# Performance work log

Measured on AMD Instinct MI355X. Metric: run time of the kernel, lower is better.

The kernel has to match this reference:

```python
import jax, jax.numpy as jnp
import numpy as np

B, S, H = 1, 2048, 2048
QL, KVL = 1536, 512
NH, NOPE, ROPE, VD = 16, 128, 64, 128
IH, ID = 16, 128
TOPK = 512
EPS = 1e-6


def _rms_norm(x, g):
    return x * jax.lax.rsqrt(jnp.mean(x * x, -1, keepdims=True) + EPS) * g


def _layer_norm(x, g, b):
    m = jnp.mean(x, -1, keepdims=True)
    v = jnp.mean((x - m) ** 2, -1, keepdims=True)
    return (x - m) * jax.lax.rsqrt(v + EPS) * g + b


def _rope(x, cos, sin):
    # x: [B,S,h,D] (D even), cos/sin: [S,D//2]; neox-style rotate-halves
    x1, x2 = jnp.split(x, 2, -1)
    c = cos[None, :, None, :]
    s = sin[None, :, None, :]
    return jnp.concatenate([x1 * c - x2 * s, x1 * s + x2 * c], -1)


def setup_inputs() -> dict:
    key = jax.random.key(0)
    ks = jax.random.split(key, 10)
    rn = lambda k, sh: (jax.random.normal(k, sh) * 0.02).astype(jnp.float32)
    pos = jnp.arange(S, dtype=jnp.float32)
    inv = 1.0 / (10000.0 ** (jnp.arange(0, ROPE, 2, dtype=jnp.float32) / ROPE))
    ang = pos[:, None] * inv[None, :]  # [S, ROPE//2]
    return {
        "hidden_states": jax.random.normal(ks[0], (B, S, H), jnp.float32),
        "cos": jnp.cos(ang),
        "sin": jnp.sin(ang),
        "Wq_a": rn(ks[1], (H, QL)),
        "q_a_gamma": jnp.ones((QL,), jnp.float32),
        "Wq_b": rn(ks[2], (QL, NH * (NOPE + ROPE))),
        "Wkv_a": rn(ks[3], (H, KVL + ROPE)),
        "kv_a_gamma": jnp.ones((KVL,), jnp.float32),
        "Wkv_b": rn(ks[4], (KVL, NH * (NOPE + VD))),
        "Wo": rn(ks[5], (NH * VD, H)),
        "Wq_idx": rn(ks[6], (QL, IH * ID)),
        "Wk_idx": rn(ks[7], (H, ID)),
        "Ww_idx": rn(ks[8], (H, IH)),
        "kn_gamma": jnp.ones((ID,), jnp.float32),
        "kn_beta": jnp.zeros((ID,), jnp.float32),
        "topk": TOPK,
    }


def reference(hidden_states, cos, sin, Wq_a, q_a_gamma, Wq_b, Wkv_a, kv_a_gamma,
              Wkv_b, Wo, Wq_idx, Wk_idx, Ww_idx, kn_gamma, kn_beta, topk):
    b, s, _ = hidden_states.shape
    softmax_scale = (NOPE + ROPE) ** -0.5

    # ---- low-rank Q path ----
    q_a = _rms_norm(hidden_states @ Wq_a, q_a_gamma)                 # [B,S,QL]
    q = (q_a @ Wq_b).reshape(b, s, NH, NOPE + ROPE)
    q_nope, q_pe = q[..., :NOPE], _rope(q[..., NOPE:], cos, sin)

    # ---- latent KV path (MQA rope key) ----
    kv = hidden_states @ Wkv_a                                        # [B,S,KVL+ROPE]
    kv_c = _rms_norm(kv[..., :KVL], kv_a_gamma)
    k_pe = _rope(kv[..., KVL:][:, :, None, :], cos, sin)[:, :, 0]     # [B,S,ROPE]
    kvb = (kv_c @ Wkv_b).reshape(b, s, NH, NOPE + VD)
    k_nope, v = kvb[..., :NOPE], kvb[..., NOPE:]

    # ---- lightning indexer: I[t,s] = sum_h w[t,h] * relu(q_idx[t,h] . k_idx[s]) ----
    qi = (q_a @ Wq_idx).reshape(b, s, IH, ID)
    qi = jnp.concatenate([_rope(qi[..., :ROPE], cos, sin), qi[..., ROPE:]], -1)
    ki = _layer_norm(hidden_states @ Wk_idx, kn_gamma, kn_beta)       # [B,S,ID]
    ki = jnp.concatenate([_rope(ki[:, :, None, :ROPE], cos, sin)[:, :, 0], ki[..., ROPE:]], -1)
    w = hidden_states @ Ww_idx                                        # [B,S,IH]
    s_h = jax.nn.relu(jnp.einsum('bthd,bsd->bhts', qi, ki)) * (ID ** -0.5)
    idx_scores = jnp.einsum('bth,bhts->bts', w, s_h)                  # [B,S,S]

    causal = jnp.tril(jnp.ones((s, s), bool))
    idx_scores = jnp.where(causal[None], idx_scores, -jnp.inf)
    top_idx = jax.lax.top_k(idx_scores, topk)[1]                      # [B,S,topk]
    sel = jnp.zeros((b, s, s), bool).at[
        jnp.arange(b)[:, None, None], jnp.arange(s)[None, :, None], top_idx
    ].set(True)
    mask = sel & causal[None]                                         # [B,S,S]

    # ---- sparse MLA attention over selected tokens ----
    scores = (jnp.einsum('bthd,bshd->bhts', q_nope, k_nope)
              + jnp.einsum('bthd,bsd->bhts', q_pe, k_pe)) * softmax_scale
    scores = jnp.where(mask[:, None], scores, -jnp.inf)
    attn = jax.nn.softmax(scores, -1)                                 # [B,NH,S,S]
    out = jnp.einsum('bhts,bshd->bthd', attn, v).reshape(b, s, NH * VD)
    return out @ Wo                                                   # [B,S,H]
```

## Files before the change

kernel.cpp:

```cpp
#include <hip/hip_runtime.h>
#include <cstdint>
#include <cstddef>
#include <cmath>

typedef unsigned long long u64;
typedef __attribute__((ext_vector_type(8))) short bf16x8;
typedef __attribute__((ext_vector_type(4))) float f32x4;

static constexpr int S_    = 2048;
static constexpr int H_    = 2048;
static constexpr int TOPKC = 512;

#define SCALE_ATTN 0.07216878364870323f
#define ISCALE_ID  0.08838834764831845f
#define EPS_F 1e-6f

__device__ inline unsigned short f2b(float f) {
  unsigned u = __float_as_uint(f);
  return (unsigned short)((u + 0x7FFFu + ((u >> 16) & 1u)) >> 16);
}
__device__ inline float b2f(unsigned short b) {
  return __uint_as_float(((unsigned)b) << 16);
}
__device__ inline void gload16(const unsigned short* g, unsigned short* l) {
  __builtin_amdgcn_global_load_lds((const __attribute__((address_space(1))) void*)g,
                                   (__attribute__((address_space(3))) void*)l, 16, 0, 0);
}

__global__ __launch_bounds__(256) void k_gemm_bf16(
    const unsigned short* __restrict__ A, int lda,
    const unsigned short* __restrict__ Bt, int K,
    void* __restrict__ C, int ldc, int N, int out_bf16) {
  __shared__ unsigned short As[128 * 64];
  __shared__ unsigned short Bs[128 * 64];
  const int bm = blockIdx.y * 128, bn = blockIdx.x * 128;
  const int tid = threadIdx.x;
  const int lane = tid & 63, w = tid >> 6;
  const int wm = w >> 1, wn = w & 1;
  const int l15 = lane & 15, quarter = lane >> 4;
  const int srow = (lane >> 3), scol = (lane & 7) * 8;

  f32x4 acc[4][4];
#pragma unroll
  for (int i = 0; i < 4; i++)
#pragma unroll
    for (int j = 0; j < 4; j++) acc[i][j] = (f32x4){0.f, 0.f, 0.f, 0.f};

  for (int k0 = 0; k0 < K; k0 += 64) {
    __syncthreads();
#pragma unroll
    for (int i = 0; i < 4; i++) {
      int r0 = w * 32 + i * 8;
      gload16(A  + (size_t)(bm + r0 + srow) * lda + k0 + scol, &As[r0 * 64]);
      gload16(Bt + (size_t)(bn + r0 + srow) * K   + k0 + scol, &Bs[r0 * 64]);
    }
    __syncthreads();
#pragma unroll
    for (int kc = 0; kc < 2; kc++) {
      bf16x8 af[4], bfr[4];
#pragma unroll
      for (int mf = 0; mf < 4; mf++)
        af[mf] = *(const bf16x8*)(As + (wm * 64 + mf * 16 + l15) * 64 + kc * 32 + quarter * 8);
#pragma unroll
      for (int nf = 0; nf < 4; nf++)
        bfr[nf] = *(const bf16x8*)(Bs + (wn * 64 + nf * 16 + l15) * 64 + kc * 32 + quarter * 8);
#pragma unroll
      for (int mf = 0; mf < 4; mf++)
#pragma unroll
        for (int nf = 0; nf < 4; nf++)
          acc[mf][nf] = __builtin_amdgcn_mfma_f32_16x16x32_bf16(af[mf], bfr[nf], acc[mf][nf], 0, 0, 0);
    }
  }
#pragma unroll
  for (int mf = 0; mf < 4; mf++)
#pragma unroll
    for (int nf = 0; nf < 4; nf++)
#pragma unroll
      for (int r = 0; r < 4; r++) {
        int grow = bm + wm * 64 + mf * 16 + quarter * 4 + r;
        int gcol = bn + wn * 64 + nf * 16 + l15;
        if (gcol < N) {
          if (out_bf16) ((unsigned short*)C)[(size_t)grow * ldc + gcol] = f2b(acc[mf][nf][r]);
          else          ((float*)C)[(size_t)grow * ldc + gcol] = acc[mf][nf][r];
        }
      }
}

__global__ __launch_bounds__(256) void k_tcast(const float* __restrict__ W, int K, int N,
                                               unsigned short* __restrict__ Wt) {
  __shared__ float T[32][33];
  int n0 = blockIdx.x * 32, k0 = blockIdx.y * 32;
  int tid = threadIdx.x;
#pragma unroll
  for (int i = 0; i < 4; i++) {
    int idx = tid + 256 * i;
    int r = idx >> 5, c = idx & 31;
    T[r][c] = W[(size_t)(k0 + r) * N + n0 + c];
  }
  __syncthreads();
#pragma unroll
  for (int i = 0; i < 4; i++) {
    int idx = tid + 256 * i;
    int r = idx >> 5, c = idx & 31;
    Wt[(size_t)(n0 + r) * K + k0 + c] = f2b(T[c][r]);
  }
}

__global__ __launch_bounds__(256) void k_tcast16(const float* __restrict__ W, int K,
                                                 unsigned short* __restrict__ Wt) {
  int idx = blockIdx.x * 256 + threadIdx.x;
  if (idx >= K * 16) return;
  int k = idx >> 4, n = idx & 15;
  Wt[(size_t)n * K + k] = f2b(W[(size_t)k * 16 + n]);
}

__global__ __launch_bounds__(256) void k_cast_bf16(const float* __restrict__ in, int pin,
                                                   unsigned short* __restrict__ outp, int pout,
                                                   int rows, int cols) {
  int cols4 = cols >> 2;
  int idx = blockIdx.x * 256 + threadIdx.x;
  if (idx >= rows * cols4) return;
  int r = idx / cols4, c = (idx - r * cols4) * 4;
  const float* ip = in + (size_t)r * pin + c;
  unsigned short* op = outp + (size_t)r * pout + c;
  op[0] = f2b(ip[0]); op[1] = f2b(ip[1]); op[2] = f2b(ip[2]); op[3] = f2b(ip[3]);
}

__global__ __launch_bounds__(256) void k_rmsnorm_cast(
    const float* __restrict__ x, int stride, const float* __restrict__ gamma,
    unsigned short* __restrict__ outp, int n) {
  int r = blockIdx.x;
  const float* p = x + (size_t)r * stride;
  __shared__ float red[256];
  float s = 0.f;
  for (int i = threadIdx.x; i < n; i += 256) { float v = p[i]; s += v * v; }
  red[threadIdx.x] = s; __syncthreads();
  for (int st = 128; st > 0; st >>= 1) { if (threadIdx.x < st) red[threadIdx.x] += red[threadIdx.x + st]; __syncthreads(); }
  float scl = rsqrtf(red[0] / (float)n + EPS_F);
  unsigned short* op = outp + (size_t)r * n;
  for (int i = threadIdx.x; i < n; i += 256) op[i] = f2b(p[i] * scl * gamma[i]);
}

__global__ __launch_bounds__(256) void k_kvfuse(
    const float* __restrict__ fat, int stride, const float* __restrict__ gamma,
    const float* __restrict__ cosb, const float* __restrict__ sinb,
    unsigned short* __restrict__ kvc_b, unsigned short* __restrict__ kpe_b) {
  int t = blockIdx.x, tid = threadIdx.x;
  const float* p = fat + (size_t)t * stride;
  __shared__ float red[256];
  float x0 = p[tid], x1 = p[tid + 256];
  red[tid] = x0 * x0 + x1 * x1; __syncthreads();
  for (int st = 128; st > 0; st >>= 1) { if (tid < st) red[tid] += red[tid + st]; __syncthreads(); }
  float scl = rsqrtf(red[0] * (1.f / 512.f) + EPS_F);
  kvc_b[(size_t)t * 512 + tid]       = f2b(x0 * scl * gamma[tid]);
  kvc_b[(size_t)t * 512 + tid + 256] = f2b(x1 * scl * gamma[tid + 256]);
  if (tid < 32) {
    float a = p[512 + tid], b = p[544 + tid];
    float c = cosb[t * 32 + tid], s = sinb[t * 32 + tid];
    kpe_b[(size_t)t * 64 + tid]      = f2b(a * c - b * s);
    kpe_b[(size_t)t * 64 + 32 + tid] = f2b(a * s + b * c);
  }
}

__global__ __launch_bounds__(128) void k_ki_ln_rope_cast(
    const float* __restrict__ ki, int stride,
    const float* __restrict__ g, const float* __restrict__ b,
    const float* __restrict__ cosb, const float* __restrict__ sinb,
    unsigned short* __restrict__ ko) {
  int t = blockIdx.x, i = threadIdx.x;
  const float* p = ki + (size_t)t * stride;
  __shared__ float red[128];
  __shared__ float buf[128];
  float v = p[i];
  red[i] = v; __syncthreads();
  for (int st = 64; st > 0; st >>= 1) { if (i < st) red[i] += red[i + st]; __syncthreads(); }
  float mean = red[0] * (1.f / 128.f);
  __syncthreads();
  float d = v - mean;
  red[i] = d * d; __syncthreads();
  for (int st = 64; st > 0; st >>= 1) { if (i < st) red[i] += red[i + st]; __syncthreads(); }
  float var = red[0] * (1.f / 128.f);
  float y = d * rsqrtf(var + EPS_F) * g[i] + b[i];
  buf[i] = y; __syncthreads();
  float outv;
  if (i < 32) {
    float c = cosb[t * 32 + i], s = sinb[t * 32 + i];
    outv = buf[i] * c - buf[i + 32] * s;
  } else if (i < 64) {
    int j = i - 32;
    float c = cosb[t * 32 + j], s = sinb[t * 32 + j];
    outv = buf[j] * s + buf[i] * c;
  } else outv = y;
  ko[(size_t)t * 128 + i] = f2b(outv);
}

__global__ __launch_bounds__(256) void k_rope_b(unsigned short* __restrict__ base, int rowstride, int nh,
                                                int hstride, int off, const float* __restrict__ cosb,
                                                const float* __restrict__ sinb, int total) {
  int idx = blockIdx.x * 256 + threadIdx.x;
  if (idx >= total) return;
  int i = idx & 31, h = (idx >> 5) % nh, t = idx / (32 * nh);
  unsigned short* p = base + (size_t)t * rowstride + h * hstride + off;
  float x1 = b2f(p[i]), x2 = b2f(p[i + 32]);
  float c = cosb[t * 32 + i], s = sinb[t * 32 + i];
  p[i] = f2b(x1 * c - x2 * s);
  p[i + 32] = f2b(x1 * s + x2 * c);
}

__global__ __launch_bounds__(256) void k_idx_mfma(
    const unsigned short* __restrict__ qi_b, int qpitch,
    const unsigned short* __restrict__ ki_b,
    const float* __restrict__ wb, int wstride,
    float* __restrict__ out) {
  int bid = blockIdx.x;
  int tb = (int)((sqrtf(8.f * bid + 1.f) - 1.f) * 0.5f);
  while ((tb + 1) * (tb + 2) / 2 <= bid) tb++;
  while (tb * (tb + 1) / 2 > bid) tb--;
  int sb = bid - tb * (tb + 1) / 2;
  int t0 = tb * 64, s0 = sb * 64;

  int tid = threadIdx.x, lane = tid & 63, w = tid >> 6;
  int wm = w >> 1, wn = w & 1;
  int l15 = lane & 15, quarter = lane >> 4;

  __shared__ unsigned short Ks[64 * 128];
  __shared__ unsigned short Qs[2][64 * 128];
  __shared__ float Ws[64][16];

  int srow_[4], scc_[4];
#pragma unroll
  for (int i = 0; i < 4; i++) {
    int row = w * 16 + i * 4 + (lane >> 4);
    int rr = row & 7;
    srow_[i] = row;
    scc_[i] = (lane & 15) ^ rr;
  }
#pragma unroll
  for (int i = 0; i < 4; i++) {
    gload16(ki_b + (size_t)(s0 + srow_[i]) * 128 + scc_[i] * 8, &Ks[(w * 16 + i * 4) * 128]);
    gload16(qi_b + (size_t)(t0 + srow_[i]) * qpitch + scc_[i] * 8, &Qs[0][(w * 16 + i * 4) * 128]);
  }
  for (int i = tid; i < 64 * 16; i += 256) Ws[i >> 4][i & 15] = wb[(size_t)(t0 + (i >> 4)) * wstride + (i & 15)];
  __syncthreads();

  bf16x8 bfr[2][4];
#pragma unroll
  for (int nf = 0; nf < 2; nf++) {
    int row = wn * 32 + nf * 16 + l15;
    int rx = (row & 7) << 3;
#pragma unroll
    for (int kc = 0; kc < 4; kc++)
      bfr[nf][kc] = *(const bf16x8*)(Ks + row * 128 + ((kc * 32 + quarter * 8) ^ rx));
  }

  f32x4 acc[2][2];
#pragma unroll
  for (int mf = 0; mf < 2; mf++)
#pragma unroll
    for (int nf = 0; nf < 2; nf++) acc[mf][nf] = (f32x4){0.f, 0.f, 0.f, 0.f};

  for (int h = 0; h < 16; h++) {
    int cur = h & 1;
    if (h < 15) {
#pragma unroll
      for (int i = 0; i < 4; i++)
        gload16(qi_b + (size_t)(t0 + srow_[i]) * qpitch + (h + 1) * 128 + scc_[i] * 8,
                &Qs[cur ^ 1][(w * 16 + i * 4) * 128]);
    }
    f32x4 acch[2][2];
#pragma unroll
    for (int mf = 0; mf < 2; mf++)
#pragma unroll
      for (int nf = 0; nf < 2; nf++) acch[mf][nf] = (f32x4){0.f, 0.f, 0.f, 0.f};

#pragma unroll
    for (int mf = 0; mf < 2; mf++) {
      int row = wm * 32 + mf * 16 + l15;
      int rx = (row & 7) << 3;
      bf16x8 af[4];
#pragma unroll
      for (int kc = 0; kc < 4; kc++)
        af[kc] = *(const bf16x8*)(Qs[cur] + row * 128 + ((kc * 32 + quarter * 8) ^ rx));
#pragma unroll
      for (int nf = 0; nf < 2; nf++)
#pragma unroll
        for (int kc = 0; kc < 4; kc++)
          acch[mf][nf] = __builtin_amdgcn_mfma_f32_16x16x32_bf16(af[kc], bfr[nf][kc], acch[mf][nf], 0, 0, 0);
    }
#pragma unroll
    for (int mf = 0; mf < 2; mf++) {
#pragma unroll
      for (int r = 0; r < 4; r++) {
        float wv = Ws[wm * 32 + mf * 16 + quarter * 4 + r][h];
#pragma unroll
        for (int nf = 0; nf < 2; nf++)
          acc[mf][nf][r] = fmaf(wv, fmaxf(acch[mf][nf][r], 0.f), acc[mf][nf][r]);
      }
    }
    __syncthreads();
  }
#pragma unroll
  for (int mf = 0; mf < 2; mf++)
#pragma unroll
    for (int nf = 0; nf < 2; nf++)
#pragma unroll
      for (int r = 0; r < 4; r++) {
        int t = t0 + wm * 32 + mf * 16 + quarter * 4 + r;
        int s = s0 + wn * 32 + nf * 16 + l15;
        out[(size_t)t * 2048 + s] = acc[mf][nf][r] * ISCALE_ID;
      }
}

__global__ __launch_bounds__(256) void k_topk_mask(const float* __restrict__ idx_sc, u64* __restrict__ maskw) {
  int t = blockIdx.x;
  int tid = threadIdx.x;
  int n = t + 1;
  if (n <= TOPKC) {
    if (tid < 32) {
      int lo = tid * 64, hi = lo + 63;
      u64 wv;
      if (t >= hi) wv = ~0ULL;
      else if (t < lo) wv = 0ULL;
      else wv = (~0ULL) >> (63 - (t - lo));
      maskw[(size_t)t * 32 + tid] = wv;
    }
    return;
  }
  __shared__ unsigned int u[2048];
  __shared__ int hist[256];
  __shared__ int scan[256];
  __shared__ u64 mw[32];
  __shared__ int sel_b, new_target, tie_base;
  __shared__ int wcnt[4];
  if (tid < 32) mw[tid] = 0ULL;
  const float* row = idx_sc + (size_t)t * 2048;
  for (int s = tid; s < n; s += 256) {
    unsigned int bb = __float_as_uint(row[s]);
    u[s] = (bb & 0x80000000u) ? ~bb : (bb | 0x80000000u);
  }
  __syncthreads();
  unsigned int prefix = 0;
  int target = TOPKC;
  for (int shift = 24; shift >= 0; shift -= 8) {
    hist[tid] = 0;
    __syncthreads();
    unsigned int himask = (shift == 24) ? 0u : (0xFFFFFFFFu << (shift + 8));
    for (int s = tid; s < n; s += 256) {
      unsigned int uv = u[s];
      if ((uv & himask) == prefix) atomicAdd(&hist[(uv >> shift) & 0xFF], 1);
    }
    __syncthreads();
    scan[tid] = hist[tid];
    __syncthreads();
#pragma unroll
    for (int st = 1; st < 256; st <<= 1) {
      int add = (tid + st < 256) ? scan[tid + st] : 0;
      __syncthreads();
      scan[tid] += add;
      __syncthreads();
    }
    int snext = (tid == 255) ? 0 : scan[tid + 1];
    if (scan[tid] >= target && snext < target) { sel_b = tid; new_target = target - snext; }
    __syncthreads();
    prefix |= ((unsigned int)sel_b) << shift;
    target = new_target;
    __syncthreads();
  }
  if (tid == 0) tie_base = 0;
  __syncthreads();
  int wid = tid >> 6, lane = tid & 63;
  for (int s0 = 0; s0 < n; s0 += 256) {
    int s = s0 + tid;
    bool in = (s < n);
    unsigned int uv = in ? u[s] : 0u;
    bool gt = in && (uv > prefix);
    bool tie = in && (uv == prefix);
    u64 bal = __ballot(tie);
    if (lane == 0) wcnt[wid] = __popcll(bal);
    __syncthreads();
    int wbase = tie_base;
    for (int wI = 0; wI < wid; wI++) wbase += wcnt[wI];
    int rank = wbase + __popcll(bal & ((1ULL << lane) - 1ULL));
    bool sel = gt || (tie && rank < target);
    if (sel) atomicOr(&mw[s >> 6], 1ULL << (s & 63));
    __syncthreads();
    if (tid == 0) tie_base += wcnt[0] + wcnt[1] + wcnt[2] + wcnt[3];
    __syncthreads();
  }
  if (tid < 32) maskw[(size_t)t * 32 + tid] = mw[tid];
}

__global__ __launch_bounds__(256) void k_attn_mfma(
    const unsigned short* __restrict__ qb, int qpitch,
    const unsigned short* __restrict__ kvb_b,
    const unsigned short* __restrict__ kpe_b,
    const float* __restrict__ cosb, const float* __restrict__ sinb,
    const u64* __restrict__ maskw,
    unsigned short* __restrict__ attn_b) {
  int ybm = blockIdx.x;
  int h = blockIdx.y;
  int yb = (h < 8) ? ybm : (31 - ybm);
  int t0 = yb * 64;
  int tid = threadIdx.x;
  int lane = tid & 63, wq = tid >> 6;
  int quarter = lane >> 4, l15 = lane & 15;

  __shared__ unsigned short Kd[2][64 * 192];
  __shared__ unsigned short Vts[128 * 64];

  const unsigned short* kb_base[6];
  int kb_step[6];
#pragma unroll
  for (int i = 0; i < 6; i++) {
    int slot = (wq * 6 + i) * 1024 + lane * 16;
    int rowk = slot / 384;
    int coff = slot - rowk * 384;
    int cc = (coff ^ ((rowk & 7) << 4)) >> 4;
    if (cc < 16) { kb_base[i] = kvb_b + (size_t)rowk * 4096 + h * 256 + cc * 8; kb_step[i] = 4096; }
    else         { kb_base[i] = kpe_b + (size_t)rowk * 64 + (cc - 16) * 8;      kb_step[i] = 64; }
  }
  const int vdg = tid & 15, vsp = tid >> 4;
  const unsigned short* vbase = kvb_b + (size_t)(vsp * 4) * 4096 + h * 256 + 128 + vdg * 8;

  bf16x8 qf[6];
  {
    int t = t0 + wq * 16 + l15;
    const unsigned short* qp = qb + (size_t)t * qpitch + h * 192 + quarter * 8;
#pragma unroll
    for (int kc = 0; kc < 6; kc++) qf[kc] = *(const bf16x8*)(qp + kc * 32);
    const float* cp = cosb + t * 32 + quarter * 8;
    const float* sp = sinb + t * 32 + quarter * 8;
    float4 ca = *(const float4*)cp,  cb2 = *(const float4*)(cp + 4);
    float4 sa = *(const float4*)sp,  sb2 = *(const float4*)(sp + 4);
    float carr[8] = {ca.x, ca.y, ca.z, ca.w, cb2.x, cb2.y, cb2.z, cb2.w};
    float sarr[8] = {sa.x, sa.y, sa.z, sa.w, sb2.x, sb2.y, sb2.z, sb2.w};
#pragma unroll
    for (int j = 0; j < 8; j++) {
      float x1 = b2f((unsigned short)qf[4][j]);
      float x2 = b2f((unsigned short)qf[5][j]);
      qf[4][j] = (short)f2b(x1 * carr[j] - x2 * sarr[j]);
      qf[5][j] = (short)f2b(x1 * sarr[j] + x2 * carr[j]);
    }
  }

  f32x4 o[8];
#pragma unroll
  for (int df = 0; df < 8; df++) o[df] = (f32x4){0.f, 0.f, 0.f, 0.f};
  float mcol = -__builtin_inff(), lcol = 0.f;
  const u64* mrow = maskw + (size_t)(t0 + wq * 16 + l15) * 32;
  int nsb = yb + 1;

#pragma unroll
  for (int i = 0; i < 6; i++) gload16(kb_base[i], &Kd[0][(wq * 6 + i) * 512]);
  bf16x8 vr0 = *(const bf16x8*)(vbase);
  bf16x8 vr1 = *(const bf16x8*)(vbase + 4096);
  bf16x8 vr2 = *(const bf16x8*)(vbase + 8192);
  bf16x8 vr3 = *(const bf16x8*)(vbase + 12288);
  __syncthreads();
#pragma unroll
  for (int j = 0; j < 8; j++) {
    int d = vdg * 8 + j;
    uint2 w2;
    w2.x = (unsigned)(unsigned short)vr0[j] | (((unsigned)(unsigned short)vr1[j]) << 16);
    w2.y = (unsigned)(unsigned short)vr2[j] | (((unsigned)(unsigned short)vr3[j]) << 16);
    *(uint2*)((char*)Vts + d * 128 + ((vsp * 8) ^ (((d >> 2) & 7) << 4))) = w2;
  }

  for (int sb = 0; sb < nsb; sb++) {
    int cur = sb & 1;
    __syncthreads();
    bool pf = (sb + 1 < nsb);
    if (pf) {
      size_t s1 = (size_t)(sb + 1) * 64;
#pragma unroll
      for (int i = 0; i < 6; i++)
        gload16(kb_base[i] + s1 * kb_step[i], &Kd[cur ^ 1][(wq * 6 + i) * 512]);
      const unsigned short* vp = vbase + s1 * 4096;
      vr0 = *(const bf16x8*)(vp);
      vr1 = *(const bf16x8*)(vp + 4096);
      vr2 = *(const bf16x8*)(vp + 8192);
      vr3 = *(const bf16x8*)(vp + 12288);
    }
    const unsigned short* Kc = Kd[cur];
    f32x4 sfT[4];
#pragma unroll
    for (int sc = 0; sc < 4; sc++) {
      f32x4 a = (f32x4){0.f, 0.f, 0.f, 0.f};
      int row = sc * 16 + l15;
      int rx = (row & 7) << 4;
#pragma unroll
      for (int kc = 0; kc < 6; kc++) {
        int byte = row * 384 + ((kc * 64 + quarter * 16) ^ rx);
        bf16x8 kf = *(const bf16x8*)((const char*)Kc + byte);
        a = __builtin_amdgcn_mfma_f32_16x16x32_bf16(kf, qf[kc], a, 0, 0, 0);
      }
      sfT[sc] = a;
    }
    u64 w64 = mrow[sb];
    float p[4][4];
#pragma unroll
    for (int sc = 0; sc < 4; sc++)
#pragma unroll
      for (int r = 0; r < 4; r++) {
        int sbit = sc * 16 + quarter * 4 + r;
        bool sel = (w64 >> sbit) & 1ULL;
        p[sc][r] = sel ? sfT[sc][r] * SCALE_ATTN : -__builtin_inff();
      }
    float v = p[0][0];
#pragma unroll
    for (int sc = 0; sc < 4; sc++)
#pragma unroll
      for (int r = 0; r < 4; r++) v = fmaxf(v, p[sc][r]);
    v = fmaxf(v, __shfl_xor(v, 16));
    v = fmaxf(v, __shfl_xor(v, 32));
    float mn = fmaxf(mcol, v);
    bool dead = (mn == -__builtin_inff());
    float scl = dead ? 1.f : __expf(mcol - mn);
#pragma unroll
    for (int sc = 0; sc < 4; sc++)
#pragma unroll
      for (int r = 0; r < 4; r++)
        p[sc][r] = dead ? 0.f : __expf(p[sc][r] - mn);
    mcol = dead ? mcol : mn;
    float rs = 0.f;
#pragma unroll
    for (int sc = 0; sc < 4; sc++)
#pragma unroll
      for (int r = 0; r < 4; r++) rs += p[sc][r];
    rs += __shfl_xor(rs, 16);
    rs += __shfl_xor(rs, 32);
    lcol = lcol * scl + rs;

    unsigned pk[4][2];
#pragma unroll
    for (int sc = 0; sc < 4; sc++)
#pragma unroll
      for (int rr = 0; rr < 2; rr++)
        pk[sc][rr] = (unsigned)f2b(p[sc][2 * rr]) | (((unsigned)f2b(p[sc][2 * rr + 1])) << 16);
    bf16x8 pa[2];
#pragma unroll
    for (int kc = 0; kc < 2; kc++) {
      union { unsigned d[4]; bf16x8 v; } pu;
#pragma unroll
      for (int jj = 0; jj < 4; jj++) {
        int src = ((quarter & 1) * 2 + (jj >> 1)) * 16 + l15;
        unsigned lo = (unsigned)__shfl((int)pk[kc * 2][jj & 1], src);
        unsigned hi = (unsigned)__shfl((int)pk[kc * 2 + 1][jj & 1], src);
        pu.d[jj] = (quarter < 2) ? lo : hi;
      }
      pa[kc] = pu.v;
    }
    float sclr[4];
#pragma unroll
    for (int r = 0; r < 4; r++) sclr[r] = __shfl(scl, quarter * 4 + r);
#pragma unroll
    for (int df = 0; df < 8; df++)
#pragma unroll
      for (int r = 0; r < 4; r++) o[df][r] *= sclr[r];
#pragma unroll
    for (int kc = 0; kc < 2; kc++)
#pragma unroll
      for (int df = 0; df < 8; df++) {
        int d = df * 16 + l15;
        int vbyte = d * 128 + ((kc * 64 + quarter * 16) ^ (((d >> 2) & 7) << 4));
        bf16x8 vf = *(const bf16x8*)((const char*)Vts + vbyte);
        o[df] = __builtin_amdgcn_mfma_f32_16x16x32_bf16(pa[kc], vf, o[df], 0, 0, 0);
      }
    __syncthreads();
    if (pf) {
#pragma unroll
      for (int j = 0; j < 8; j++) {
        int d = vdg * 8 + j;
        uint2 w2;
        w2.x = (unsigned)(unsigned short)vr0[j] | (((unsigned)(unsigned short)vr1[j]) << 16);
        w2.y = (unsigned)(unsigned short)vr2[j] | (((unsigned)(unsigned short)vr3[j]) << 16);
        *(uint2*)((char*)Vts + d * 128 + ((vsp * 8) ^ (((d >> 2) & 7) << 4))) = w2;
      }
    }
  }
  float inv = (lcol > 0.f) ? 1.f / lcol : 0.f;
  float invr[4];
#pragma unroll
  for (int r = 0; r < 4; r++) invr[r] = __shfl(inv, quarter * 4 + r);
#pragma unroll
  for (int r = 0; r < 4; r++) {
    int t = t0 + wq * 16 + quarter * 4 + r;
    unsigned short* op = attn_b + (size_t)t * 2048 + h * 128 + l15;
#pragma unroll
    for (int df = 0; df < 8; df++) op[df * 16] = f2b(o[df][r] * invr[r]);
  }
}

extern "C" void kernel_launch(void* const* d_in, const int* in_sizes, int n_in,
                              void* d_out, int out_size, void* d_ws, size_t ws_size,
                              hipStream_t stream) {
  const float* hs     = (const float*)d_in[0];
  const float* cosb   = (const float*)d_in[1];
  const float* sinb   = (const float*)d_in[2];
  const float* Wq_a   = (const float*)d_in[3];
  const float* q_a_g  = (const float*)d_in[4];
  const float* Wq_b   = (const float*)d_in[5];
  const float* Wkv_a  = (const float*)d_in[6];
  const float* kv_a_g = (const float*)d_in[7];
  const float* Wkv_b  = (const float*)d_in[8];
  const float* Wo     = (const float*)d_in[9];
  const float* Wq_idx = (const float*)d_in[10];
  const float* Wk_idx = (const float*)d_in[11];
  const float* Ww_idx = (const float*)d_in[12];
  const float* kn_g   = (const float*)d_in[13];
  const float* kn_b   = (const float*)d_in[14];
  float* out = (float*)d_out;

  char* base = (char*)d_ws;
  size_t off = 0;
  auto alloc = [&](size_t bytes) { void* p = base + off; off += (bytes + 255) & ~size_t(255); return p; };

  float* fat1 = (float*)alloc((size_t)S_ * 2304 * 4);
  float* idxs = (float*)alloc((size_t)S_ * 2048 * 4);
  unsigned short* attn_b = (unsigned short*)idxs;
  unsigned short* fat2 = (unsigned short*)alloc((size_t)S_ * 5120 * 2);
  u64*   maskw = (u64*)alloc((size_t)S_ * 32 * 8);
  unsigned short* hs_b  = (unsigned short*)alloc((size_t)S_ * 2048 * 2);
  unsigned short* qa_b  = (unsigned short*)alloc((size_t)S_ * 1536 * 2);
  unsigned short* kvc_b = (unsigned short*)alloc((size_t)S_ * 512 * 2);
  unsigned short* kpe_b = (unsigned short*)alloc((size_t)S_ * 64 * 2);
  unsigned short* kvb_b = (unsigned short*)alloc((size_t)S_ * 4096 * 2);
  unsigned short* ki_b  = (unsigned short*)alloc((size_t)S_ * 128 * 2);
  unsigned short* WT    = (unsigned short*)alloc((size_t)5120 * 1536 * 2);

  dim3 blk(256);

  k_cast_bf16<<<dim3((S_ * 2048 / 4) / 256), blk, 0, stream>>>(hs, 2048, hs_b, 2048, S_, 2048);
  k_tcast<<<dim3(1536 / 32, 2048 / 32), blk, 0, stream>>>(Wq_a, 2048, 1536, WT);
  k_tcast<<<dim3(576 / 32, 2048 / 32), blk, 0, stream>>>(Wkv_a, 2048, 576, WT + (size_t)1536 * 2048);
  k_tcast<<<dim3(128 / 32, 2048 / 32), blk, 0, stream>>>(Wk_idx, 2048, 128, WT + (size_t)2112 * 2048);
  k_tcast16<<<dim3((2048 * 16) / 256), blk, 0, stream>>>(Ww_idx, 2048, WT + (size_t)2240 * 2048);
  k_gemm_bf16<<<dim3(18, 16), blk, 0, stream>>>(hs_b, 2048, WT, 2048, fat1, 2304, 2256, 0);
  k_rmsnorm_cast<<<dim3(S_), blk, 0, stream>>>(fat1, 2304, q_a_g, qa_b, 1536);
  k_kvfuse<<<dim3(S_), blk, 0, stream>>>(fat1 + 1536, 2304, kv_a_g, cosb, sinb, kvc_b, kpe_b);
  k_ki_ln_rope_cast<<<dim3(S_), dim3(128), 0, stream>>>(fat1 + 2112, 2304, kn_g, kn_b, cosb, sinb, ki_b);
  k_tcast<<<dim3(3072 / 32, 1536 / 32), blk, 0, stream>>>(Wq_b, 1536, 3072, WT);
  k_tcast<<<dim3(2048 / 32, 1536 / 32), blk, 0, stream>>>(Wq_idx, 1536, 2048, WT + (size_t)3072 * 1536);
  k_gemm_bf16<<<dim3(40, 16), blk, 0, stream>>>(qa_b, 1536, WT, 1536, fat2, 5120, 5120, 1);
  k_rope_b<<<dim3((S_ * 16 * 32) / 256), blk, 0, stream>>>(fat2 + 3072, 5120, 16, 128, 0, cosb, sinb, S_ * 16 * 32);
  k_tcast<<<dim3(4096 / 32, 512 / 32), blk, 0, stream>>>(Wkv_b, 512, 4096, WT);
  k_gemm_bf16<<<dim3(32, 16), blk, 0, stream>>>(kvc_b, 512, WT, 512, kvb_b, 4096, 4096, 1);
  k_idx_mfma<<<dim3(528), blk, 0, stream>>>(fat2 + 3072, 5120, ki_b, fat1 + 2240, 2304, idxs);
  k_topk_mask<<<dim3(S_), blk, 0, stream>>>(idxs, maskw);
  k_attn_mfma<<<dim3(32, 16), blk, 0, stream>>>(fat2, 5120, kvb_b, kpe_b, cosb, sinb, maskw, attn_b);
  k_tcast<<<dim3(2048 / 32, 2048 / 32), blk, 0, stream>>>(Wo, 2048, 2048, WT);
  k_gemm_bf16<<<dim3(16, 16), blk, 0, stream>>>(attn_b, 2048, WT, 2048, out, 2048, 2048, 0);

  (void)in_sizes; (void)n_in; (void)out_size; (void)ws_size;
}
```

Before: 368.0 us.

## Split attention KV range into two partitions with merge; fuse transposes and norms

```diff
diff --git a/kernel.cpp b/kernel.cpp
--- a/kernel.cpp
+++ b/kernel.cpp
@@ -86,32 +86,58 @@
       }
 }
 
-__global__ __launch_bounds__(256) void k_tcast(const float* __restrict__ W, int K, int N,
-                                               unsigned short* __restrict__ Wt) {
-  __shared__ float T[32][33];
-  int n0 = blockIdx.x * 32, k0 = blockIdx.y * 32;
-  int tid = threadIdx.x;
+__device__ inline void tcast_tile(const float* __restrict__ W, int K, int N,
+                                  unsigned short* __restrict__ dst,
+                                  int r, int ntx, int tid, float (*T)[33]) {
+  int xt = r % ntx, kt = r / ntx;
+  int n0 = xt * 32, k0 = kt * 32;
 #pragma unroll
   for (int i = 0; i < 4; i++) {
     int idx = tid + 256 * i;
-    int r = idx >> 5, c = idx & 31;
-    T[r][c] = W[(size_t)(k0 + r) * N + n0 + c];
+    int rr = idx >> 5, c = idx & 31;
+    T[rr][c] = W[(size_t)(k0 + rr) * N + n0 + c];
   }
   __syncthreads();
 #pragma unroll
   for (int i = 0; i < 4; i++) {
     int idx = tid + 256 * i;
-    int r = idx >> 5, c = idx & 31;
-    Wt[(size_t)(n0 + r) * K + k0 + c] = f2b(T[c][r]);
-  }
-}
-
-__global__ __launch_bounds__(256) void k_tcast16(const float* __restrict__ W, int K,
-                                                 unsigned short* __restrict__ Wt) {
-  int idx = blockIdx.x * 256 + threadIdx.x;
-  if (idx >= K * 16) return;
-  int k = idx >> 4, n = idx & 15;
-  Wt[(size_t)n * K + k] = f2b(W[(size_t)k * 16 + n]);
+    int rr = idx >> 5, c = idx & 31;
+    dst[(size_t)(n0 + rr) * K + k0 + c] = f2b(T[c][rr]);
+  }
+}
+
+__global__ __launch_bounds__(256) void k_tcast_p1(
+    const float* __restrict__ Wq_a, const float* __restrict__ Wkv_a,
+    const float* __restrict__ Wk_idx, const float* __restrict__ Ww_idx,
+    unsigned short* __restrict__ WT) {
+  __shared__ float T[32][33];
+  int bid = blockIdx.x, tid = threadIdx.x;
+  if (bid < 3072)      tcast_tile(Wq_a,  2048, 1536, WT,                          bid,        48, tid, T);
+  else if (bid < 4224) tcast_tile(Wkv_a, 2048,  576, WT + (size_t)1536 * 2048,    bid - 3072, 18, tid, T);
+  else if (bid < 4480) tcast_tile(Wk_idx,2048,  128, WT + (size_t)2112 * 2048,    bid - 4224,  4, tid, T);
+  else {
+    int idx = (bid - 4480) * 256 + tid;
+    int k = idx >> 4, n = idx & 15;
+    WT[(size_t)(2240 + n) * 2048 + k] = f2b(Ww_idx[(size_t)k * 16 + n]);
+  }
+}
+
+__global__ __launch_bounds__(256) void k_tcast_p2(
+    const float* __restrict__ Wq_b, const float* __restrict__ Wq_idx,
+    unsigned short* __restrict__ WT) {
+  __shared__ float T[32][33];
+  int bid = blockIdx.x, tid = threadIdx.x;
+  if (bid < 4608) tcast_tile(Wq_b,   1536, 3072, WT,                        bid,        96, tid, T);
+  else            tcast_tile(Wq_idx, 1536, 2048, WT + (size_t)3072 * 1536,  bid - 4608, 64, tid, T);
+}
+
+__global__ __launch_bounds__(256) void k_tcast_p3(
+    const float* __restrict__ Wkv_b, const float* __restrict__ Wo,
+    unsigned short* __restrict__ WT) {
+  __shared__ float T[32][33];
+  int bid = blockIdx.x, tid = threadIdx.x;
+  if (bid < 2048) tcast_tile(Wkv_b,  512, 4096, WT,                       bid,        128, tid, T);
+  else            tcast_tile(Wo,    2048, 2048, WT + (size_t)4096 * 512,  bid - 2048,  64, tid, T);
 }
 
 __global__ __launch_bounds__(256) void k_cast_bf16(const float* __restrict__ in, int pin,
@@ -126,72 +152,63 @@
   op[0] = f2b(ip[0]); op[1] = f2b(ip[1]); op[2] = f2b(ip[2]); op[3] = f2b(ip[3]);
 }
 
-__global__ __launch_bounds__(256) void k_rmsnorm_cast(
-    const float* __restrict__ x, int stride, const float* __restrict__ gamma,
-    unsigned short* __restrict__ outp, int n) {
-  int r = blockIdx.x;
-  const float* p = x + (size_t)r * stride;
-  __shared__ float red[256];
-  float s = 0.f;
-  for (int i = threadIdx.x; i < n; i += 256) { float v = p[i]; s += v * v; }
-  red[threadIdx.x] = s; __syncthreads();
-  for (int st = 128; st > 0; st >>= 1) { if (threadIdx.x < st) red[threadIdx.x] += red[threadIdx.x + st]; __syncthreads(); }
-  float scl = rsqrtf(red[0] / (float)n + EPS_F);
-  unsigned short* op = outp + (size_t)r * n;
-  for (int i = threadIdx.x; i < n; i += 256) op[i] = f2b(p[i] * scl * gamma[i]);
-}
-
-__global__ __launch_bounds__(256) void k_kvfuse(
-    const float* __restrict__ fat, int stride, const float* __restrict__ gamma,
+__global__ __launch_bounds__(256) void k_norms(
+    const float* __restrict__ fat, int stride,
+    const float* __restrict__ qg, const float* __restrict__ kvg,
+    const float* __restrict__ kng, const float* __restrict__ knb,
     const float* __restrict__ cosb, const float* __restrict__ sinb,
-    unsigned short* __restrict__ kvc_b, unsigned short* __restrict__ kpe_b) {
+    unsigned short* __restrict__ qa_b, unsigned short* __restrict__ kvc_b,
+    unsigned short* __restrict__ kpe_b, unsigned short* __restrict__ ki_b) {
   int t = blockIdx.x, tid = threadIdx.x;
   const float* p = fat + (size_t)t * stride;
   __shared__ float red[256];
-  float x0 = p[tid], x1 = p[tid + 256];
-  red[tid] = x0 * x0 + x1 * x1; __syncthreads();
+  __shared__ float buf[128];
+  float x[6]; float s = 0.f;
+#pragma unroll
+  for (int i = 0; i < 6; i++) { x[i] = p[tid + 256 * i]; s += x[i] * x[i]; }
+  red[tid] = s; __syncthreads();
   for (int st = 128; st > 0; st >>= 1) { if (tid < st) red[tid] += red[tid + st]; __syncthreads(); }
-  float scl = rsqrtf(red[0] * (1.f / 512.f) + EPS_F);
-  kvc_b[(size_t)t * 512 + tid]       = f2b(x0 * scl * gamma[tid]);
-  kvc_b[(size_t)t * 512 + tid + 256] = f2b(x1 * scl * gamma[tid + 256]);
+  float scl = rsqrtf(red[0] * (1.f / 1536.f) + EPS_F);
+#pragma unroll
+  for (int i = 0; i < 6; i++)
+    qa_b[(size_t)t * 1536 + tid + 256 * i] = f2b(x[i] * scl * qg[tid + 256 * i]);
+  __syncthreads();
+  float y0 = p[1536 + tid], y1 = p[1792 + tid];
+  red[tid] = y0 * y0 + y1 * y1; __syncthreads();
+  for (int st = 128; st > 0; st >>= 1) { if (tid < st) red[tid] += red[tid + st]; __syncthreads(); }
+  float scl2 = rsqrtf(red[0] * (1.f / 512.f) + EPS_F);
+  kvc_b[(size_t)t * 512 + tid]       = f2b(y0 * scl2 * kvg[tid]);
+  kvc_b[(size_t)t * 512 + 256 + tid] = f2b(y1 * scl2 * kvg[256 + tid]);
   if (tid < 32) {
-    float a = p[512 + tid], b = p[544 + tid];
-    float c = cosb[t * 32 + tid], s = sinb[t * 32 + tid];
-    kpe_b[(size_t)t * 64 + tid]      = f2b(a * c - b * s);
-    kpe_b[(size_t)t * 64 + 32 + tid] = f2b(a * s + b * c);
-  }
-}
-
-__global__ __launch_bounds__(128) void k_ki_ln_rope_cast(
-    const float* __restrict__ ki, int stride,
-    const float* __restrict__ g, const float* __restrict__ b,
-    const float* __restrict__ cosb, const float* __restrict__ sinb,
-    unsigned short* __restrict__ ko) {
-  int t = blockIdx.x, i = threadIdx.x;
-  const float* p = ki + (size_t)t * stride;
-  __shared__ float red[128];
-  __shared__ float buf[128];
-  float v = p[i];
-  red[i] = v; __syncthreads();
-  for (int st = 64; st > 0; st >>= 1) { if (i < st) red[i] += red[i + st]; __syncthreads(); }
+    float a = p[2048 + tid], b = p[2080 + tid];
+    float c = cosb[t * 32 + tid], sn = sinb[t * 32 + tid];
+    kpe_b[(size_t)t * 64 + tid]      = f2b(a * c - b * sn);
+    kpe_b[(size_t)t * 64 + 32 + tid] = f2b(a * sn + b * c);
+  }
+  __syncthreads();
+  float z = (tid < 128) ? p[2112 + tid] : 0.f;
+  red[tid] = z; __syncthreads();
+  for (int st = 128; st > 0; st >>= 1) { if (tid < st) red[tid] += red[tid + st]; __syncthreads(); }
   float mean = red[0] * (1.f / 128.f);
   __syncthreads();
-  float d = v - mean;
-  red[i] = d * d; __syncthreads();
-  for (int st = 64; st > 0; st >>= 1) { if (i < st) red[i] += red[i + st]; __syncthreads(); }
+  float d = (tid < 128) ? (z - mean) : 0.f;
+  red[tid] = d * d; __syncthreads();
+  for (int st = 128; st > 0; st >>= 1) { if (tid < st) red[tid] += red[tid + st]; __syncthreads(); }
   float var = red[0] * (1.f / 128.f);
-  float y = d * rsqrtf(var + EPS_F) * g[i] + b[i];
-  buf[i] = y; __syncthreads();
-  float outv;
-  if (i < 32) {
-    float c = cosb[t * 32 + i], s = sinb[t * 32 + i];
-    outv = buf[i] * c - buf[i + 32] * s;
-  } else if (i < 64) {
-    int j = i - 32;
-    float c = cosb[t * 32 + j], s = sinb[t * 32 + j];
-    outv = buf[j] * s + buf[i] * c;
-  } else outv = y;
-  ko[(size_t)t * 128 + i] = f2b(outv);
+  if (tid < 128) buf[tid] = d * rsqrtf(var + EPS_F) * kng[tid] + knb[tid];
+  __syncthreads();
+  if (tid < 128) {
+    float outv;
+    if (tid < 32) {
+      float c = cosb[t * 32 + tid], sn = sinb[t * 32 + tid];
+      outv = buf[tid] * c - buf[tid + 32] * sn;
+    } else if (tid < 64) {
+      int j = tid - 32;
+      float c = cosb[t * 32 + j], sn = sinb[t * 32 + j];
+      outv = buf[j] * sn + buf[tid] * c;
+    } else outv = buf[tid];
+    ki_b[(size_t)t * 128 + tid] = f2b(outv);
+  }
 }
 
 __global__ __launch_bounds__(256) void k_rope_b(unsigned short* __restrict__ base, int rowstride, int nh,
@@ -231,9 +248,8 @@
 #pragma unroll
   for (int i = 0; i < 4; i++) {
     int row = w * 16 + i * 4 + (lane >> 4);
-    int rr = row & 7;
     srow_[i] = row;
-    scc_[i] = (lane & 15) ^ rr;
+    scc_[i] = (lane & 15) ^ (row & 7);
   }
 #pragma unroll
   for (int i = 0; i < 4; i++) {
@@ -273,6 +289,7 @@
 #pragma unroll
       for (int nf = 0; nf < 2; nf++) acch[mf][nf] = (f32x4){0.f, 0.f, 0.f, 0.f};
 
+    __builtin_amdgcn_s_setprio(1);
 #pragma unroll
     for (int mf = 0; mf < 2; mf++) {
       int row = wm * 32 + mf * 16 + l15;
@@ -287,6 +304,7 @@
         for (int kc = 0; kc < 4; kc++)
           acch[mf][nf] = __builtin_amdgcn_mfma_f32_16x16x32_bf16(af[kc], bfr[nf][kc], acch[mf][nf], 0, 0, 0);
     }
+    __builtin_amdgcn_s_setprio(0);
 #pragma unroll
     for (int mf = 0; mf < 2; mf++) {
 #pragma unroll
@@ -396,23 +414,25 @@
     const unsigned short* __restrict__ kpe_b,
     const float* __restrict__ cosb, const float* __restrict__ sinb,
     const u64* __restrict__ maskw,
-    unsigned short* __restrict__ attn_b) {
+    unsigned short* __restrict__ opart,
+    float* __restrict__ mlbuf) {
   int ybm = blockIdx.x;
   int h = blockIdx.y;
+  int ph = blockIdx.z;
   int yb = (h < 8) ? ybm : (31 - ybm);
   int t0 = yb * 64;
   int tid = threadIdx.x;
   int lane = tid & 63, wq = tid >> 6;
   int quarter = lane >> 4, l15 = lane & 15;
 
-  __shared__ unsigned short Kd[2][64 * 192];
-  __shared__ unsigned short Vts[128 * 64];
-
-  const unsigned short* kb_base[6];
-  int kb_step[6];
-#pragma unroll
-  for (int i = 0; i < 6; i++) {
-    int slot = (wq * 6 + i) * 1024 + lane * 16;
+  __shared__ unsigned short Kd[2][32 * 192];
+  __shared__ unsigned short Vts[128 * 32];
+
+  const unsigned short* kb_base[3];
+  int kb_step[3];
+#pragma unroll
+  for (int i = 0; i < 3; i++) {
+    int slot = (wq * 3 + i) * 1024 + lane * 16;
     int rowk = slot / 384;
     int coff = slot - rowk * 384;
     int cc = (coff ^ ((rowk & 7) << 4)) >> 4;
@@ -420,7 +440,7 @@
     else         { kb_base[i] = kpe_b + (size_t)rowk * 64 + (cc - 16) * 8;      kb_step[i] = 64; }
   }
   const int vdg = tid & 15, vsp = tid >> 4;
-  const unsigned short* vbase = kvb_b + (size_t)(vsp * 4) * 4096 + h * 256 + 128 + vdg * 8;
+  const unsigned short* vbase = kvb_b + (size_t)(vsp * 2) * 4096 + h * 256 + 128 + vdg * 8;
 
   bf16x8 qf[6];
   {
@@ -448,43 +468,42 @@
   for (int df = 0; df < 8; df++) o[df] = (f32x4){0.f, 0.f, 0.f, 0.f};
   float mcol = -__builtin_inff(), lcol = 0.f;
   const u64* mrow = maskw + (size_t)(t0 + wq * 16 + l15) * 32;
-  int nsb = yb + 1;
-
-#pragma unroll
-  for (int i = 0; i < 6; i++) gload16(kb_base[i], &Kd[0][(wq * 6 + i) * 512]);
-  bf16x8 vr0 = *(const bf16x8*)(vbase);
-  bf16x8 vr1 = *(const bf16x8*)(vbase + 4096);
-  bf16x8 vr2 = *(const bf16x8*)(vbase + 8192);
-  bf16x8 vr3 = *(const bf16x8*)(vbase + 12288);
+  int ntile = 2 * yb + 2;
+
+  {
+    size_t sr = (size_t)ph * 32;
+#pragma unroll
+    for (int i = 0; i < 3; i++) gload16(kb_base[i] + sr * kb_step[i], &Kd[0][(wq * 3 + i) * 512]);
+  }
+  bf16x8 vr0 = *(const bf16x8*)(vbase + (size_t)ph * 32 * 4096);
+  bf16x8 vr1 = *(const bf16x8*)(vbase + (size_t)(ph * 32 + 1) * 4096);
   __syncthreads();
 #pragma unroll
   for (int j = 0; j < 8; j++) {
     int d = vdg * 8 + j;
-    uint2 w2;
-    w2.x = (unsigned)(unsigned short)vr0[j] | (((unsigned)(unsigned short)vr1[j]) << 16);
-    w2.y = (unsigned)(unsigned short)vr2[j] | (((unsigned)(unsigned short)vr3[j]) << 16);
-    *(uint2*)((char*)Vts + d * 128 + ((vsp * 8) ^ (((d >> 2) & 7) << 4))) = w2;
-  }
-
-  for (int sb = 0; sb < nsb; sb++) {
-    int cur = sb & 1;
-    __syncthreads();
-    bool pf = (sb + 1 < nsb);
+    unsigned pack = (unsigned)(unsigned short)vr0[j] | (((unsigned)(unsigned short)vr1[j]) << 16);
+    *(unsigned*)((char*)Vts + d * 64 + ((vsp * 4) ^ ((d & 3) << 4))) = pack;
+  }
+
+  int cur = 0;
+  for (int k = ph; k < ntile; k += 2) {
+    __syncthreads();
+    bool pf = (k + 2 < ntile);
     if (pf) {
-      size_t s1 = (size_t)(sb + 1) * 64;
-#pragma unroll
-      for (int i = 0; i < 6; i++)
-        gload16(kb_base[i] + s1 * kb_step[i], &Kd[cur ^ 1][(wq * 6 + i) * 512]);
-      const unsigned short* vp = vbase + s1 * 4096;
-      vr0 = *(const bf16x8*)(vp);
+      size_t sn = (size_t)(k + 2) * 32;
+#pragma unroll
+      for (int i = 0; i < 3; i++)
+        gload16(kb_base[i] + sn * kb_step[i], &Kd[cur ^ 1][(wq * 3 + i) * 512]);
+      const unsigned short* vp = vbase + sn * 4096;
+      vr0 = *(const bf16x8*)vp;
       vr1 = *(const bf16x8*)(vp + 4096);
-      vr2 = *(const bf16x8*)(vp + 8192);
-      vr3 = *(const bf16x8*)(vp + 12288);
-    }
+    }
+    int s0 = k * 32;
     const unsigned short* Kc = Kd[cur];
-    f32x4 sfT[4];
-#pragma unroll
-    for (int sc = 0; sc < 4; sc++) {
+    f32x4 sfT[2];
+    __builtin_amdgcn_s_setprio(1);
+#pragma unroll
+    for (int sc = 0; sc < 2; sc++) {
       f32x4 a = (f32x4){0.f, 0.f, 0.f, 0.f};
       int row = sc * 16 + l15;
       int rx = (row & 7) << 4;
@@ -496,99 +515,132 @@
       }
       sfT[sc] = a;
     }
-    u64 w64 = mrow[sb];
-    float p[4][4];
-#pragma unroll
-    for (int sc = 0; sc < 4; sc++)
+    __builtin_amdgcn_s_setprio(0);
+    u64 w64 = mrow[s0 >> 6];
+    int shiftb = s0 & 32;
+    float p[2][4];
+#pragma unroll
+    for (int sc = 0; sc < 2; sc++)
 #pragma unroll
       for (int r = 0; r < 4; r++) {
-        int sbit = sc * 16 + quarter * 4 + r;
+        int sbit = shiftb + sc * 16 + quarter * 4 + r;
         bool sel = (w64 >> sbit) & 1ULL;
         p[sc][r] = sel ? sfT[sc][r] * SCALE_ATTN : -__builtin_inff();
       }
     float v = p[0][0];
-#pragma unroll
-    for (int sc = 0; sc < 4; sc++)
-#pragma unroll
-      for (int r = 0; r < 4; r++) v = fmaxf(v, p[sc][r]);
+    v = fmaxf(v, p[0][1]); v = fmaxf(v, p[0][2]); v = fmaxf(v, p[0][3]);
+    v = fmaxf(v, p[1][0]); v = fmaxf(v, p[1][1]); v = fmaxf(v, p[1][2]); v = fmaxf(v, p[1][3]);
     v = fmaxf(v, __shfl_xor(v, 16));
     v = fmaxf(v, __shfl_xor(v, 32));
-    float mn = fmaxf(mcol, v);
-    bool dead = (mn == -__builtin_inff());
-    float scl = dead ? 1.f : __expf(mcol - mn);
-#pragma unroll
-    for (int sc = 0; sc < 4; sc++)
-#pragma unroll
-      for (int r = 0; r < 4; r++)
-        p[sc][r] = dead ? 0.f : __expf(p[sc][r] - mn);
-    mcol = dead ? mcol : mn;
-    float rs = 0.f;
-#pragma unroll
-    for (int sc = 0; sc < 4; sc++)
-#pragma unroll
-      for (int r = 0; r < 4; r++) rs += p[sc][r];
+    bool need = __any(v > mcol + 8.f);
+    float scl = 1.f;
+    if (need) {
+      float mn = fmaxf(mcol, v);
+      bool dead = (mn == -__builtin_inff());
+      scl = dead ? 1.f : __expf(mcol - mn);
+#pragma unroll
+      for (int sc = 0; sc < 2; sc++)
+#pragma unroll
+        for (int r = 0; r < 4; r++)
+          p[sc][r] = dead ? 0.f : __expf(p[sc][r] - mn);
+      mcol = dead ? mcol : mn;
+    } else {
+      float basem = (mcol == -__builtin_inff()) ? 0.f : mcol;
+#pragma unroll
+      for (int sc = 0; sc < 2; sc++)
+#pragma unroll
+        for (int r = 0; r < 4; r++)
+          p[sc][r] = __expf(p[sc][r] - basem);
+    }
+    float rs = p[0][0] + p[0][1] + p[0][2] + p[0][3] + p[1][0] + p[1][1] + p[1][2] + p[1][3];
     rs += __shfl_xor(rs, 16);
     rs += __shfl_xor(rs, 32);
     lcol = lcol * scl + rs;
 
-    unsigned pk[4][2];
-#pragma unroll
-    for (int sc = 0; sc < 4; sc++)
-#pragma unroll
-      for (int rr = 0; rr < 2; rr++)
-        pk[sc][rr] = (unsigned)f2b(p[sc][2 * rr]) | (((unsigned)f2b(p[sc][2 * rr + 1])) << 16);
-    bf16x8 pa[2];
-#pragma unroll
-    for (int kc = 0; kc < 2; kc++) {
-      union { unsigned d[4]; bf16x8 v; } pu;
-#pragma unroll
-      for (int jj = 0; jj < 4; jj++) {
-        int src = ((quarter & 1) * 2 + (jj >> 1)) * 16 + l15;
-        unsigned lo = (unsigned)__shfl((int)pk[kc * 2][jj & 1], src);
-        unsigned hi = (unsigned)__shfl((int)pk[kc * 2 + 1][jj & 1], src);
-        pu.d[jj] = (quarter < 2) ? lo : hi;
-      }
-      pa[kc] = pu.v;
-    }
-    float sclr[4];
-#pragma unroll
-    for (int r = 0; r < 4; r++) sclr[r] = __shfl(scl, quarter * 4 + r);
-#pragma unroll
-    for (int df = 0; df < 8; df++)
-#pragma unroll
-      for (int r = 0; r < 4; r++) o[df][r] *= sclr[r];
-#pragma unroll
-    for (int kc = 0; kc < 2; kc++)
-#pragma unroll
-      for (int df = 0; df < 8; df++) {
-        int d = df * 16 + l15;
-        int vbyte = d * 128 + ((kc * 64 + quarter * 16) ^ (((d >> 2) & 7) << 4));
-        bf16x8 vf = *(const bf16x8*)((const char*)Vts + vbyte);
-        o[df] = __builtin_amdgcn_mfma_f32_16x16x32_bf16(pa[kc], vf, o[df], 0, 0, 0);
-      }
+    unsigned pk0[2], pk1[2];
+#pragma unroll
+    for (int rr = 0; rr < 2; rr++) {
+      pk0[rr] = (unsigned)f2b(p[0][2 * rr]) | (((unsigned)f2b(p[0][2 * rr + 1])) << 16);
+      pk1[rr] = (unsigned)f2b(p[1][2 * rr]) | (((unsigned)f2b(p[1][2 * rr + 1])) << 16);
+    }
+    union { unsigned d[4]; bf16x8 v; } pu;
+#pragma unroll
+    for (int jj = 0; jj < 4; jj++) {
+      int src = ((quarter & 1) * 2 + (jj >> 1)) * 16 + l15;
+      unsigned a0 = (unsigned)__shfl((int)pk0[jj & 1], src);
+      unsigned a1 = (unsigned)__shfl((int)pk1[jj & 1], src);
+      pu.d[jj] = (quarter < 2) ? a0 : a1;
+    }
+    bf16x8 pa = pu.v;
+
+    if (need) {
+      float sclr[4];
+#pragma unroll
+      for (int r = 0; r < 4; r++) sclr[r] = __shfl(scl, quarter * 4 + r);
+#pragma unroll
+      for (int df = 0; df < 8; df++)
+#pragma unroll
+        for (int r = 0; r < 4; r++) o[df][r] *= sclr[r];
+    }
+    __builtin_amdgcn_s_setprio(1);
+#pragma unroll
+    for (int df = 0; df < 8; df++) {
+      int d = df * 16 + l15;
+      int vbyte = d * 64 + ((quarter * 16) ^ ((d & 3) << 4));
+      bf16x8 vf = *(const bf16x8*)((const char*)Vts + vbyte);
+      o[df] = __builtin_amdgcn_mfma_f32_16x16x32_bf16(pa, vf, o[df], 0, 0, 0);
+    }
+    __builtin_amdgcn_s_setprio(0);
     __syncthreads();
     if (pf) {
 #pragma unroll
       for (int j = 0; j < 8; j++) {
         int d = vdg * 8 + j;
-        uint2 w2;
-        w2.x = (unsigned)(unsigned short)vr0[j] | (((unsigned)(unsigned short)vr1[j]) << 16);
-        w2.y = (unsigned)(unsigned short)vr2[j] | (((unsigned)(unsigned short)vr3[j]) << 16);
-        *(uint2*)((char*)Vts + d * 128 + ((vsp * 8) ^ (((d >> 2) & 7) << 4))) = w2;
+        unsigned pack = (unsigned)(unsigned short)vr0[j] | (((unsigned)(unsigned short)vr1[j]) << 16);
+        *(unsigned*)((char*)Vts + d * 64 + ((vsp * 4) ^ ((d & 3) << 4))) = pack;
       }
     }
-  }
-  float inv = (lcol > 0.f) ? 1.f / lcol : 0.f;
-  float invr[4];
-#pragma unroll
-  for (int r = 0; r < 4; r++) invr[r] = __shfl(inv, quarter * 4 + r);
+    cur ^= 1;
+  }
+  unsigned short* ob = opart + (size_t)ph * S_ * 2048;
 #pragma unroll
   for (int r = 0; r < 4; r++) {
     int t = t0 + wq * 16 + quarter * 4 + r;
-    unsigned short* op = attn_b + (size_t)t * 2048 + h * 128 + l15;
-#pragma unroll
-    for (int df = 0; df < 8; df++) op[df * 16] = f2b(o[df][r] * invr[r]);
-  }
+    unsigned short* op = ob + (size_t)t * 2048 + h * 128 + l15;
+#pragma unroll
+    for (int df = 0; df < 8; df++) op[df * 16] = f2b(o[df][r]);
+  }
+  if (quarter == 0) {
+    int t = t0 + wq * 16 + l15;
+    float* mp = mlbuf + ((size_t)ph * S_ * 16 + (size_t)t * 16 + h) * 2;
+    mp[0] = mcol;
+    mp[1] = lcol;
+  }
+}
+
+__global__ __launch_bounds__(256) void k_attn_merge(
+    const unsigned short* __restrict__ opart, const float* __restrict__ mlbuf,
+    unsigned short* __restrict__ attn_b) {
+  int idx = blockIdx.x * 256 + threadIdx.x;
+  int dg = idx & 15, h = (idx >> 4) & 15, t = idx >> 8;
+  const float* ml0 = mlbuf + ((size_t)t * 16 + h) * 2;
+  const float* ml1 = ml0 + (size_t)S_ * 16 * 2;
+  float m0 = ml0[0], l0 = ml0[1];
+  float m1 = ml1[0], l1 = ml1[1];
+  float m = fmaxf(m0, m1);
+  float w0 = (m0 == -__builtin_inff()) ? 0.f : __expf(m0 - m);
+  float w1 = (m1 == -__builtin_inff()) ? 0.f : __expf(m1 - m);
+  float L = l0 * w0 + l1 * w1;
+  float inv = (L > 0.f) ? 1.f / L : 0.f;
+  const bf16x8 o0 = *(const bf16x8*)(opart + (size_t)t * 2048 + h * 128 + dg * 8);
+  const bf16x8 o1 = *(const bf16x8*)(opart + (size_t)S_ * 2048 + (size_t)t * 2048 + h * 128 + dg * 8);
+  bf16x8 r;
+#pragma unroll
+  for (int j = 0; j < 8; j++) {
+    float a = b2f((unsigned short)o0[j]) * w0 + b2f((unsigned short)o1[j]) * w1;
+    r[j] = (short)f2b(a * inv);
+  }
+  *(bf16x8*)(attn_b + (size_t)t * 2048 + h * 128 + dg * 8) = r;
 }
 
 extern "C" void kernel_launch(void* const* d_in, const int* in_sizes, int n_in,
@@ -616,9 +668,11 @@
   auto alloc = [&](size_t bytes) { void* p = base + off; off += (bytes + 255) & ~size_t(255); return p; };
 
   float* fat1 = (float*)alloc((size_t)S_ * 2304 * 4);
+  unsigned short* attn_b = (unsigned short*)fat1;
   float* idxs = (float*)alloc((size_t)S_ * 2048 * 4);
-  unsigned short* attn_b = (unsigned short*)idxs;
+  unsigned short* opart = (unsigned short*)idxs;
   unsigned short* fat2 = (unsigned short*)alloc((size_t)S_ * 5120 * 2);
+  float* mlbuf = (float*)alloc((size_t)2 * S_ * 16 * 2 * 4);
   u64*   maskw = (u64*)alloc((size_t)S_ * 32 * 8);
   unsigned short* hs_b  = (unsigned short*)alloc((size_t)S_ * 2048 * 2);
   unsigned short* qa_b  = (unsigned short*)alloc((size_t)S_ * 1536 * 2);
@@ -631,25 +685,21 @@
   dim3 blk(256);
 
   k_cast_bf16<<<dim3((S_ * 2048 / 4) / 256), blk, 0, stream>>>(hs, 2048, hs_b, 2048, S_, 2048);
-  k_tcast<<<dim3(1536 / 32, 2048 / 32), blk, 0, stream>>>(Wq_a, 2048, 1536, WT);
-  k_tcast<<<dim3(576 / 32, 2048 / 32), blk, 0, stream>>>(Wkv_a, 2048, 576, WT + (size_t)1536 * 2048);
-  k_tcast<<<dim3(128 / 32, 2048 / 32), blk, 0, stream>>>(Wk_idx, 2048, 128, WT + (size_t)2112 * 2048);
-  k_tcast16<<<dim3((2048 * 16) / 256), blk, 0, stream>>>(Ww_idx, 2048, WT + (size_t)2240 * 2048);
+  k_tcast_p1<<<dim3(4608), blk, 0, stream>>>(Wq_a, Wkv_a, Wk_idx, Ww_idx, WT);
   k_gemm_bf16<<<dim3(18, 16), blk, 0, stream>>>(hs_b, 2048, WT, 2048, fat1, 2304, 2256, 0);
-  k_rmsnorm_cast<<<dim3(S_), blk, 0, stream>>>(fat1, 2304, q_a_g, qa_b, 1536);
-  k_kvfuse<<<dim3(S_), blk, 0, stream>>>(fat1 + 1536, 2304, kv_a_g, cosb, sinb, kvc_b, kpe_b);
-  k_ki_ln_rope_cast<<<dim3(S_), dim3(128), 0, stream>>>(fat1 + 2112, 2304, kn_g, kn_b, cosb, sinb, ki_b);
-  k_tcast<<<dim3(3072 / 32, 1536 / 32), blk, 0, stream>>>(Wq_b, 1536, 3072, WT);
-  k_tcast<<<dim3(2048 / 32, 1536 / 32), blk, 0, stream>>>(Wq_idx, 1536, 2048, WT + (size_t)3072 * 1536);
+  k_norms<<<dim3(S_), blk, 0, stream>>>(fat1, 2304, q_a_g, kv_a_g, kn_g, kn_b, cosb, sinb,
+                                        qa_b, kvc_b, kpe_b, ki_b);
+  k_tcast_p2<<<dim3(7680), blk, 0, stream>>>(Wq_b, Wq_idx, WT);
   k_gemm_bf16<<<dim3(40, 16), blk, 0, stream>>>(qa_b, 1536, WT, 1536, fat2, 5120, 5120, 1);
   k_rope_b<<<dim3((S_ * 16 * 32) / 256), blk, 0, stream>>>(fat2 + 3072, 5120, 16, 128, 0, cosb, sinb, S_ * 16 * 32);
-  k_tcast<<<dim3(4096 / 32, 512 / 32), blk, 0, stream>>>(Wkv_b, 512, 4096, WT);
+  k_tcast_p3<<<dim3(6144), blk, 0, stream>>>(Wkv_b, Wo, WT);
   k_gemm_bf16<<<dim3(32, 16), blk, 0, stream>>>(kvc_b, 512, WT, 512, kvb_b, 4096, 4096, 1);
   k_idx_mfma<<<dim3(528), blk, 0, stream>>>(fat2 + 3072, 5120, ki_b, fat1 + 2240, 2304, idxs);
   k_topk_mask<<<dim3(S_), blk, 0, stream>>>(idxs, maskw);
-  k_attn_mfma<<<dim3(32, 16), blk, 0, stream>>>(fat2, 5120, kvb_b, kpe_b, cosb, sinb, maskw, attn_b);
-  k_tcast<<<dim3(2048 / 32, 2048 / 32), blk, 0, stream>>>(Wo, 2048, 2048, WT);
-  k_gemm_bf16<<<dim3(16, 16), blk, 0, stream>>>(attn_b, 2048, WT, 2048, out, 2048, 2048, 0);
+  k_attn_mfma<<<dim3(32, 16, 2), blk, 0, stream>>>(fat2, 5120, kvb_b, kpe_b, cosb, sinb, maskw,
+                                                   opart, mlbuf);
+  k_attn_merge<<<dim3((S_ * 16 * 16) / 256), blk, 0, stream>>>(opart, mlbuf, attn_b);
+  k_gemm_bf16<<<dim3(16, 16), blk, 0, stream>>>(attn_b, 2048, WT + (size_t)4096 * 512, 2048, out, 2048, 2048, 0);
 
   (void)in_sizes; (void)n_in; (void)out_size; (void)ws_size;
 }
```

After: 380.4 us. 3.4% more time.
